# Kernel tuning notes

Measured on AMD Instinct MI355X. Metric: run time of the kernel, lower is better.

The kernel has to match this reference:

```python
import jax, jax.numpy as jnp
import numpy as np

NEG_SLOPE = 0.1

def lrelu(x):
    return jnp.where(x > 0, x, NEG_SLOPE * x)

def conv3(x, w, b):
    # 3x3 conv, stride 1, pad 1, NCHW / OIHW
    y = jax.lax.conv_general_dilated(x, w, (1, 1), ((1, 1), (1, 1)),
                                     dimension_numbers=('NCHW', 'OIHW', 'NCHW'))
    return y + b[None, :, None, None]

def correlation(f1, f2, stride):
    # 7x7 windowed cost volume, displacements in {-3..3}*stride, zero pad, /C
    B, C, H, W = f1.shape
    pad = 3 * stride
    f1s = f1[:, :, ::stride, ::stride]                      # [B,C,Ho,Wo] (ceil)
    f2p = jnp.pad(f2, ((0, 0), (0, 0), (pad, pad), (pad, pad)))
    outs = []
    for dy in range(7):
        for dx in range(7):
            sl = f2p[:, :, dy * stride: dy * stride + H: stride,
                           dx * stride: dx * stride + W: stride]
            outs.append(jnp.sum(f1s * sl, axis=1))           # [B,Ho,Wo]
    return jnp.stack(outs, axis=1) / C                       # [B,49,Ho,Wo]

def apply_offset(offset):
    # offset: [B,2,H,W]; channel 0 = x displacement, 1 = y displacement
    B, _, H, W = offset.shape
    gx = jnp.arange(W, dtype=offset.dtype)[None, None, :] + offset[:, 0]
    gy = jnp.arange(H, dtype=offset.dtype)[None, :, None] + offset[:, 1]
    gx = gx / ((W - 1.0) / 2.0) - 1.0
    gy = gy / ((H - 1.0) / 2.0) - 1.0
    return jnp.stack([gx, gy], axis=-1)                      # [B,H,W,2]

def grid_sample(img, grid):
    # bilinear, padding_mode='border', align_corners=True
    B, C, H, W = img.shape
    x = jnp.clip((grid[..., 0] + 1.0) * 0.5 * (W - 1), 0.0, W - 1.0)
    y = jnp.clip((grid[..., 1] + 1.0) * 0.5 * (H - 1), 0.0, H - 1.0)
    x0 = jnp.floor(x); y0 = jnp.floor(y)
    wx = x - x0; wy = y - y0
    x0 = x0.astype(jnp.int32); y0 = y0.astype(jnp.int32)
    x1 = jnp.minimum(x0 + 1, W - 1); y1 = jnp.minimum(y0 + 1, H - 1)
    imgf = img.reshape(B, C, H * W)
    def gather(yy, xx):
        idx = (yy * W + xx).reshape(B, 1, H * W)
        g = jnp.take_along_axis(imgf, jnp.broadcast_to(idx, (B, C, H * W)), axis=2)
        return g.reshape(B, C, H, W)
    wx = wx[:, None]; wy = wy[:, None]
    return (gather(y0, x0) * (1 - wx) * (1 - wy) + gather(y0, x1) * wx * (1 - wy)
            + gather(y1, x0) * (1 - wx) * wy + gather(y1, x1) * wx * wy)

def setup_inputs() -> dict:
    key = jax.random.key(0)
    ks = jax.random.split(key, 12)
    B, C, H, W = 8, 256, 128, 96
    s = 0.05
    return {
        'feat1': jax.random.normal(ks[0], (B, C, H, W), jnp.float32),
        'feat2': jax.random.normal(ks[1], (B, C, H, W), jnp.float32),
        'w1': s * jax.random.normal(ks[2], (128, 49, 3, 3), jnp.float32),
        'b1': jnp.zeros((128,), jnp.float32),
        'w2': s * jax.random.normal(ks[3], (64, 128, 3, 3), jnp.float32),
        'b2': jnp.zeros((64,), jnp.float32),
        'w3': s * jax.random.normal(ks[4], (32, 64, 3, 3), jnp.float32),
        'b3': jnp.zeros((32,), jnp.float32),
        'w4': s * jax.random.normal(ks[5], (2, 32, 3, 3), jnp.float32),
        'b4': jnp.zeros((2,), jnp.float32),
        'stride': 1,
    }

def reference(feat1, feat2, w1, b1, w2, b2, w3, b3, w4, b4, stride):
    corr = lrelu(correlation(feat1, feat2, stride))          # [B,49,H,W]
    h = lrelu(conv3(corr, w1, b1))
    h = lrelu(conv3(h, w2, b2))
    h = lrelu(conv3(h, w3, b3))
    flow = conv3(h, w4, b4)                                  # [B,2,H,W]
    grid = apply_offset(flow)
    warped = grid_sample(feat2, grid)                        # [B,C,H,W]
    return warped
```

## Files before the change

### kernel.cpp

```cpp
#include <hip/hip_runtime.h>

constexpr int B_ = 8, C_ = 256, H_ = 128, W_ = 96;
constexpr int HW_ = H_ * W_;

typedef __bf16 bf16x8 __attribute__((ext_vector_type(8)));
typedef float f32x4 __attribute__((ext_vector_type(4)));

__device__ __forceinline__ float lrelu_f(float v) { return v > 0.f ? v : 0.1f * v; }
__device__ __forceinline__ ushort f2b(float v) {
    __bf16 h = (__bf16)v;
    return __builtin_bit_cast(ushort, h);
}
__device__ __forceinline__ float blo(unsigned u) {
    return __builtin_bit_cast(float, u << 16);
}
__device__ __forceinline__ float bhi(unsigned u) {
    return __builtin_bit_cast(float, u & 0xffff0000u);
}

constexpr int CR = 4;
constexpr int F2R = 12;
constexpr int CCH = 8;

__global__ __launch_bounds__(768)
void corr_kernel(const float* __restrict__ f1, const float* __restrict__ f2,
                 ushort* __restrict__ corr_nhwc)
{
    __shared__ __align__(16) float s2[F2R][CCH][128];
    __shared__ __align__(16) float s1[CCH][CR][96];

    const int tid = threadIdx.x;
    const int pxg = tid % 24;
    const int ty = (tid / 24) % CR;
    const int dy = tid / 96;
    const int x0 = pxg * 4;

    const int b = blockIdx.x >> 5;
    const int y0 = (blockIdx.x & 31) * CR;

    float acc[7][4];
#pragma unroll
    for (int j = 0; j < 7; j++)
#pragma unroll
        for (int k = 0; k < 4; k++) acc[j][k] = 0.f;

    const float* f1p = f1 + b * C_ * HW_;
    const float* f2p = f2 + b * C_ * HW_;

    for (int cc = 0; cc < C_; cc += CCH) {
        __syncthreads();
#pragma unroll
        for (int k = 0; k < 16; k++) {
            int e = k * 768 + tid;
            int col = e & 127;
            int c = (e >> 7) & 7;
            int r = e >> 10;
            int yg = y0 + r - 3;
            int xg = col - 3;
            bool valid = ((unsigned)yg < (unsigned)H_) && ((unsigned)xg < (unsigned)W_);
            int ygc = min(max(yg, 0), H_ - 1);
            int xgc = min(max(xg, 0), W_ - 1);
            float v = f2p[(cc + c) * HW_ + ygc * W_ + xgc];
            s2[r][c][col] = valid ? v : 0.f;
        }
#pragma unroll
        for (int k = 0; k < 4; k++) {
            int e = k * 768 + tid;
            int idx = e / 96;
            int col = e - idx * 96;
            int c = idx >> 2;
            int r = idx & 3;
            s1[c][r][col] = f1p[(cc + c) * HW_ + (y0 + r) * W_ + col];
        }
        __syncthreads();
#pragma unroll
        for (int c = 0; c < CCH; c++) {
            float4 v1 = *(const float4*)&s1[c][ty][x0];
            float v1a[4] = {v1.x, v1.y, v1.z, v1.w};
            const float* rp = &s2[ty + dy][c][x0];
            float4 a0 = *(const float4*)&rp[0];
            float4 a1 = *(const float4*)&rp[4];
            float4 a2 = *(const float4*)&rp[8];
            float iv[12] = {a0.x, a0.y, a0.z, a0.w, a1.x, a1.y, a1.z, a1.w,
                            a2.x, a2.y, a2.z, a2.w};
#pragma unroll
            for (int dx = 0; dx < 7; dx++)
#pragma unroll
                for (int p = 0; p < 4; p++)
                    acc[dx][p] += v1a[p] * iv[p + dx];
        }
    }

    __syncthreads();
    ushort* t = (ushort*)&s2[0][0][0];
    const float scale = 1.f / 256.f;
    if (dy < 7) {
#pragma unroll
        for (int dx = 0; dx < 7; dx++)
#pragma unroll
            for (int p = 0; p < 4; p++)
                t[(ty * 96 + x0 + p) * 64 + dy * 7 + dx] =
                    f2b(lrelu_f(acc[dx][p] * scale));
    } else {
#pragma unroll
        for (int p = 0; p < 4; p++)
            for (int c = 49; c < 64; c++)
                t[(ty * 96 + x0 + p) * 64 + c] = 0;
    }
    __syncthreads();
    const uint4* src = (const uint4*)t;
    uint4* dst = (uint4*)(corr_nhwc + (size_t)(b * HW_ + y0 * W_) * 64);
    for (int e = tid; e < 3072; e += 768) dst[e] = src[e];
}

template <int CIN, int COUT, int CIP>
__global__ __launch_bounds__(256)
void pack_w(const float* __restrict__ w, ushort* __restrict__ wpk)
{
    int i = blockIdx.x * 256 + threadIdx.x;
    if (i >= 9 * COUT * CIP) return;
    int ci = i % CIP;
    int t = i / CIP;
    int oc = t % COUT;
    int tap = t / COUT;
    float v = (ci < CIN) ? w[(oc * CIN + ci) * 9 + tap] : 0.f;
    wpk[i] = f2b(v);
}

template <int CIP, int COUT, int OCB, int XT, int XTILES>
__global__ __launch_bounds__(256)
void conv_mfma(const ushort* __restrict__ in, const ushort* __restrict__ wpk,
               const float* __restrict__ bias, ushort* __restrict__ out)
{
    constexpr int OCF = OCB / 16, PXF = XT / 16, COLS = XT + 2;
    constexpr int G = CIP / 8, KC = CIP / 32;
    __shared__ __align__(16) ushort sIn[6 * COLS * CIP];

    const int tid = threadIdx.x;
    const int lane = tid & 63;
    const int ty = tid >> 6;
    const int ln = lane & 15;
    const int lq = lane >> 4;

    const int gx = blockIdx.x;
    const int xt = gx % XTILES;
    const int yt = (gx / XTILES) % 32;
    const int b = gx / (XTILES * 32);
    const int oc0 = blockIdx.y * OCB;
    const int x0 = xt * XT;
    const int y0 = yt * 4;

    constexpr int NU = 6 * COLS * G;
    for (int e = tid; e < NU; e += 256) {
        int g = e & (G - 1);
        int pc = e / G;
        int col = pc % COLS;
        int rr = pc / COLS;
        int yg = y0 - 1 + rr;
        int xg = x0 - 1 + col;
        uint4 v = make_uint4(0, 0, 0, 0);
        if ((unsigned)yg < (unsigned)H_ && (unsigned)xg < (unsigned)W_)
            v = *(const uint4*)(in + ((size_t)(b * HW_ + yg * W_ + xg) * CIP + g * 8));
        int p = rr * COLS + col;
        *(uint4*)(sIn + (size_t)(p * G + (g ^ (p & 7))) * 8) = v;
    }
    __syncthreads();

    f32x4 acc[OCF][PXF];
#pragma unroll
    for (int of = 0; of < OCF; of++)
#pragma unroll
        for (int pf = 0; pf < PXF; pf++) {
            f32x4 z = {0.f, 0.f, 0.f, 0.f};
            acc[of][pf] = z;
        }

    const uint4* wq = (const uint4*)wpk;
    for (int kc = 0; kc < KC; kc++) {
        for (int tap = 0; tap < 9; tap++) {
            const int r = tap / 3, s = tap % 3;
            bf16x8 afr[OCF];
#pragma unroll
            for (int of = 0; of < OCF; of++) {
                int off = ((tap * COUT + oc0 + of * 16 + ln) * CIP + kc * 32 + lq * 8) >> 3;
                afr[of] = __builtin_bit_cast(bf16x8, wq[off]);
            }
#pragma unroll
            for (int pf = 0; pf < PXF; pf++) {
                int p = (ty + r) * COLS + (pf * 16 + ln + s);
                int g = kc * 4 + lq;
                uint4 bv = *(const uint4*)(sIn + (size_t)(p * G + (g ^ (p & 7))) * 8);
                bf16x8 bfr = __builtin_bit_cast(bf16x8, bv);
#pragma unroll
                for (int of = 0; of < OCF; of++)
                    acc[of][pf] = __builtin_amdgcn_mfma_f32_16x16x32_bf16(
                        afr[of], bfr, acc[of][pf], 0, 0, 0);
            }
        }
    }

    const int y = y0 + ty;
#pragma unroll
    for (int of = 0; of < OCF; of++) {
        int ocb = oc0 + of * 16 + lq * 4;
        float4 bv = *(const float4*)(bias + ocb);
        float bs[4] = {bv.x, bv.y, bv.z, bv.w};
#pragma unroll
        for (int pf = 0; pf < PXF; pf++) {
            int x = x0 + pf * 16 + ln;
            ushort4 pk;
            pk.x = f2b(lrelu_f(acc[of][pf][0] + bs[0]));
            pk.y = f2b(lrelu_f(acc[of][pf][1] + bs[1]));
            pk.z = f2b(lrelu_f(acc[of][pf][2] + bs[2]));
            pk.w = f2b(lrelu_f(acc[of][pf][3] + bs[3]));
            *(ushort4*)(out + ((size_t)(b * HW_ + y * W_ + x) * COUT + ocb)) = pk;
        }
    }
}

__global__ __launch_bounds__(256)
void conv4_kernel(const ushort* __restrict__ in, const float* __restrict__ wgt,
                  const float* __restrict__ bias, float* __restrict__ flow)
{
    __shared__ float s_w[2 * 9 * 32];
    const int tid = threadIdx.x;
    for (int e = tid; e < 576; e += 256) {
        int ci = e & 31;
        int t = e >> 5;
        int tap = t % 9;
        int oc = t / 9;
        s_w[e] = wgt[(oc * 32 + ci) * 9 + tap];
    }
    __syncthreads();

    int pix = blockIdx.x * 256 + tid;
    int b = pix / HW_;
    int rem = pix - b * HW_;
    int yy = rem / W_;
    int xx = rem - yy * W_;

    float a0 = bias[0], a1 = bias[1];
    for (int tap = 0; tap < 9; tap++) {
        int r = tap / 3, s = tap % 3;
        int yg = yy + r - 1, xg = xx + s - 1;
        if ((unsigned)yg >= (unsigned)H_ || (unsigned)xg >= (unsigned)W_) continue;
        const uint4* p = (const uint4*)(in + (size_t)(b * HW_ + yg * W_ + xg) * 32);
        const float* w0 = &s_w[(0 * 9 + tap) * 32];
        const float* w1 = &s_w[(1 * 9 + tap) * 32];
#pragma unroll
        for (int q = 0; q < 4; q++) {
            uint4 v = p[q];
            unsigned uu[4] = {v.x, v.y, v.z, v.w};
#pragma unroll
            for (int h = 0; h < 4; h++) {
                int ci = q * 8 + h * 2;
                float vl = blo(uu[h]), vh = bhi(uu[h]);
                a0 += vl * w0[ci] + vh * w0[ci + 1];
                a1 += vl * w1[ci] + vh * w1[ci + 1];
            }
        }
    }
    flow[(b * 2 + 0) * HW_ + rem] = a0;
    flow[(b * 2 + 1) * HW_ + rem] = a1;
}

__global__ __launch_bounds__(256)
void warp_kernel(const float* __restrict__ f2, const float* __restrict__ flow,
                 float* __restrict__ out)
{
    int pix = blockIdx.x * 256 + threadIdx.x;
    int b = pix / HW_;
    int rem = pix - b * HW_;
    int yy = rem / W_;
    int xx = rem - yy * W_;

    float fx = flow[(b * 2 + 0) * HW_ + rem];
    float fy = flow[(b * 2 + 1) * HW_ + rem];
    float xs = fminf(fmaxf((float)xx + fx, 0.f), (float)(W_ - 1));
    float ys = fminf(fmaxf((float)yy + fy, 0.f), (float)(H_ - 1));
    float x0f = floorf(xs), y0f = floorf(ys);
    int x0 = (int)x0f, y0 = (int)y0f;
    float wx = xs - x0f, wy = ys - y0f;
    int x1 = min(x0 + 1, W_ - 1), y1 = min(y0 + 1, H_ - 1);

    int i00 = y0 * W_ + x0, i01 = y0 * W_ + x1;
    int i10 = y1 * W_ + x0, i11 = y1 * W_ + x1;
    float w00 = (1.f - wx) * (1.f - wy), w01 = wx * (1.f - wy);
    float w10 = (1.f - wx) * wy, w11 = wx * wy;

    const float* base = f2 + b * C_ * HW_;
    float* ob = out + b * C_ * HW_ + rem;
#pragma unroll 4
    for (int c = 0; c < C_; c++) {
        const float* p = base + c * HW_;
        ob[c * HW_] = p[i00] * w00 + p[i01] * w01 + p[i10] * w10 + p[i11] * w11;
    }
}

extern "C" void kernel_launch(void* const* d_in, const int* in_sizes, int n_in,
                              void* d_out, int out_size, void* d_ws, size_t ws_size,
                              hipStream_t stream)
{
    (void)in_sizes; (void)n_in; (void)out_size; (void)ws_size;
    const float* feat1 = (const float*)d_in[0];
    const float* feat2 = (const float*)d_in[1];
    const float* w1 = (const float*)d_in[2];
    const float* b1 = (const float*)d_in[3];
    const float* w2 = (const float*)d_in[4];
    const float* b2 = (const float*)d_in[5];
    const float* w3 = (const float*)d_in[6];
    const float* b3 = (const float*)d_in[7];
    const float* w4 = (const float*)d_in[8];
    const float* b4 = (const float*)d_in[9];

    char* ws = (char*)d_ws;
    ushort* corr_nhwc = (ushort*)(ws);
    ushort* h1 = (ushort*)(ws + 12582912);
    ushort* h2 = (ushort*)(ws + 37748736);
    ushort* h3 = (ushort*)(ws + 50331648);
    float* flow = (float*)(ws + 56623104);
    ushort* wpk1 = (ushort*)(ws + 57409536);
    ushort* wpk2 = (ushort*)(ws + 57556992);
    ushort* wpk3 = (ushort*)(ws + 57704448);
    float* out = (float*)d_out;

    pack_w<49, 128, 64><<<288, 256, 0, stream>>>(w1, wpk1);
    pack_w<128, 64, 128><<<288, 256, 0, stream>>>(w2, wpk2);
    pack_w<64, 32, 64><<<72, 256, 0, stream>>>(w3, wpk3);

    corr_kernel<<<256, 768, 0, stream>>>(feat1, feat2, corr_nhwc);
    conv_mfma<64, 128, 64, 48, 2><<<dim3(512, 2), 256, 0, stream>>>(corr_nhwc, wpk1, b1, h1);
    conv_mfma<128, 64, 64, 32, 3><<<dim3(768, 1), 256, 0, stream>>>(h1, wpk2, b2, h2);
    conv_mfma<64, 32, 32, 48, 2><<<dim3(512, 1), 256, 0, stream>>>(h2, wpk3, b3, h3);
    conv4_kernel<<<384, 256, 0, stream>>>(h3, w4, b4, flow);
    warp_kernel<<<384, 256, 0, stream>>>(feat2, flow, out);
}
```

Baseline: 522.2 us.

## Prefetch correlation tiles into registers, shrink row tiles, split warp over channels

The correlation kernel now processes 2 output rows per block with 384 threads (512 blocks) instead of 4 rows with 768. It loads the next channel chunk of feat1/feat2 into registers while computing the current one, which overlaps global loads with FMA work. Global offsets are precomputed once, shared-memory strides are padded to cut bank conflicts, and a block-index swizzle spreads work across batches. The warp kernel is split into 4 channel groups to quadruple the grid, at the cost of recomputing the bilinear indices per group and using more registers in the correlation kernel.

```diff
diff --git a/kernel.cpp b/kernel.cpp
--- a/kernel.cpp
+++ b/kernel.cpp
@@ -18,81 +18,125 @@
     return __builtin_bit_cast(float, u & 0xffff0000u);
 }
 
-constexpr int CR = 4;
-constexpr int F2R = 12;
 constexpr int CCH = 8;
-
-__global__ __launch_bounds__(768)
+constexpr int ROWS = 8;
+constexpr int SCOLS = 108;
+constexpr int S2STR = 132;
+constexpr int S1STR = 100;
+constexpr int NS2 = ROWS * CCH * SCOLS;
+constexpr int NPT2 = NS2 / 384;
+constexpr int NS1 = CCH * 2 * 96;
+constexpr int NPT1 = NS1 / 384;
+
+__global__ __launch_bounds__(384)
 void corr_kernel(const float* __restrict__ f1, const float* __restrict__ f2,
                  ushort* __restrict__ corr_nhwc)
 {
-    __shared__ __align__(16) float s2[F2R][CCH][128];
-    __shared__ __align__(16) float s1[CCH][CR][96];
+    __shared__ __align__(16) float s2f[CCH * ROWS * S2STR];
+    __shared__ __align__(16) float s1f[CCH * 2 * S1STR];
 
     const int tid = threadIdx.x;
     const int pxg = tid % 24;
-    const int ty = (tid / 24) % CR;
-    const int dy = tid / 96;
+    const int ty = (tid / 24) & 1;
+    const int dy = tid / 48;
     const int x0 = pxg * 4;
 
-    const int b = blockIdx.x >> 5;
-    const int y0 = (blockIdx.x & 31) * CR;
-
-    float acc[7][4];
-#pragma unroll
-    for (int j = 0; j < 7; j++)
-#pragma unroll
-        for (int k = 0; k < 4; k++) acc[j][k] = 0.f;
+    const int bid = blockIdx.x;
+    const int wg = (bid & 7) * 64 + (bid >> 3);
+    const int b = wg >> 6;
+    const int y0 = (wg & 63) * 2;
+
+    int goff2[NPT2], la2[NPT2];
+    unsigned gm = 0;
+#pragma unroll
+    for (int i = 0; i < NPT2; i++) {
+        int e = tid + i * 384;
+        int col = e % SCOLS;
+        int idx = e / SCOLS;
+        int c = idx & (CCH - 1);
+        int rr = idx >> 3;
+        int yg = y0 + rr - 3;
+        int xg = col - 3;
+        bool v = ((unsigned)yg < (unsigned)H_) && ((unsigned)xg < (unsigned)W_);
+        gm |= (unsigned)v << i;
+        int ygc = min(max(yg, 0), H_ - 1);
+        int xgc = min(max(xg, 0), W_ - 1);
+        goff2[i] = c * HW_ + ygc * W_ + xgc;
+        la2[i] = (c * ROWS + rr) * S2STR + col;
+    }
+    int goff1[NPT1], la1[NPT1];
+#pragma unroll
+    for (int i = 0; i < NPT1; i++) {
+        int e = tid + i * 384;
+        int col = e % 96;
+        int idx = e / 96;
+        int c = idx >> 1;
+        int tt = idx & 1;
+        goff1[i] = c * HW_ + (y0 + tt) * W_ + col;
+        la1[i] = (c * 2 + tt) * S1STR + col;
+    }
 
     const float* f1p = f1 + b * C_ * HW_;
     const float* f2p = f2 + b * C_ * HW_;
 
+    float acc[7][4];
+#pragma unroll
+    for (int j = 0; j < 7; j++)
+#pragma unroll
+        for (int k = 0; k < 4; k++) acc[j][k] = 0.f;
+
+    float r2[NPT2], r1[NPT1];
+#pragma unroll
+    for (int i = 0; i < NPT2; i++) {
+        float v = f2p[goff2[i]];
+        r2[i] = ((gm >> i) & 1u) ? v : 0.f;
+    }
+#pragma unroll
+    for (int i = 0; i < NPT1; i++) r1[i] = f1p[goff1[i]];
+
     for (int cc = 0; cc < C_; cc += CCH) {
         __syncthreads();
 #pragma unroll
-        for (int k = 0; k < 16; k++) {
-            int e = k * 768 + tid;
-            int col = e & 127;
-            int c = (e >> 7) & 7;
-            int r = e >> 10;
-            int yg = y0 + r - 3;
-            int xg = col - 3;
-            bool valid = ((unsigned)yg < (unsigned)H_) && ((unsigned)xg < (unsigned)W_);
-            int ygc = min(max(yg, 0), H_ - 1);
-            int xgc = min(max(xg, 0), W_ - 1);
-            float v = f2p[(cc + c) * HW_ + ygc * W_ + xgc];
-            s2[r][c][col] = valid ? v : 0.f;
-        }
-#pragma unroll
-        for (int k = 0; k < 4; k++) {
-            int e = k * 768 + tid;
-            int idx = e / 96;
-            int col = e - idx * 96;
-            int c = idx >> 2;
-            int r = idx & 3;
-            s1[c][r][col] = f1p[(cc + c) * HW_ + (y0 + r) * W_ + col];
-        }
+        for (int i = 0; i < NPT2; i++) s2f[la2[i]] = r2[i];
+#pragma unroll
+        for (int i = 0; i < NPT1; i++) s1f[la1[i]] = r1[i];
         __syncthreads();
-#pragma unroll
-        for (int c = 0; c < CCH; c++) {
-            float4 v1 = *(const float4*)&s1[c][ty][x0];
-            float v1a[4] = {v1.x, v1.y, v1.z, v1.w};
-            const float* rp = &s2[ty + dy][c][x0];
-            float4 a0 = *(const float4*)&rp[0];
-            float4 a1 = *(const float4*)&rp[4];
-            float4 a2 = *(const float4*)&rp[8];
-            float iv[12] = {a0.x, a0.y, a0.z, a0.w, a1.x, a1.y, a1.z, a1.w,
-                            a2.x, a2.y, a2.z, a2.w};
-#pragma unroll
-            for (int dx = 0; dx < 7; dx++)
-#pragma unroll
-                for (int p = 0; p < 4; p++)
-                    acc[dx][p] += v1a[p] * iv[p + dx];
+
+        if (cc + CCH < C_) {
+            const float* f2n = f2p + (cc + CCH) * HW_;
+            const float* f1n = f1p + (cc + CCH) * HW_;
+#pragma unroll
+            for (int i = 0; i < NPT2; i++) {
+                float v = f2n[goff2[i]];
+                r2[i] = ((gm >> i) & 1u) ? v : 0.f;
+            }
+#pragma unroll
+            for (int i = 0; i < NPT1; i++) r1[i] = f1n[goff1[i]];
+        }
+
+        if (dy < 7) {
+            const int r = ty + dy;
+#pragma unroll
+            for (int c = 0; c < CCH; c++) {
+                float4 v1 = *(const float4*)&s1f[(c * 2 + ty) * S1STR + x0];
+                float v1a[4] = {v1.x, v1.y, v1.z, v1.w};
+                const float* rp = &s2f[(c * ROWS + r) * S2STR + x0];
+                float4 a0 = *(const float4*)&rp[0];
+                float4 a1 = *(const float4*)&rp[4];
+                float4 a2 = *(const float4*)&rp[8];
+                float iv[12] = {a0.x, a0.y, a0.z, a0.w, a1.x, a1.y, a1.z, a1.w,
+                                a2.x, a2.y, a2.z, a2.w};
+#pragma unroll
+                for (int dx = 0; dx < 7; dx++)
+#pragma unroll
+                    for (int p = 0; p < 4; p++)
+                        acc[dx][p] += v1a[p] * iv[p + dx];
+            }
         }
     }
 
     __syncthreads();
-    ushort* t = (ushort*)&s2[0][0][0];
+    ushort* t = (ushort*)s2f;
     const float scale = 1.f / 256.f;
     if (dy < 7) {
 #pragma unroll
@@ -110,7 +154,8 @@
     __syncthreads();
     const uint4* src = (const uint4*)t;
     uint4* dst = (uint4*)(corr_nhwc + (size_t)(b * HW_ + y0 * W_) * 64);
-    for (int e = tid; e < 3072; e += 768) dst[e] = src[e];
+#pragma unroll
+    for (int k = 0; k < 4; k++) dst[k * 384 + tid] = src[k * 384 + tid];
 }
 
 template <int CIN, int COUT, int CIP>
@@ -269,6 +314,7 @@
                  float* __restrict__ out)
 {
     int pix = blockIdx.x * 256 + threadIdx.x;
+    int cbase = blockIdx.y * 64;
     int b = pix / HW_;
     int rem = pix - b * HW_;
     int yy = rem / W_;
@@ -288,10 +334,10 @@
     float w00 = (1.f - wx) * (1.f - wy), w01 = wx * (1.f - wy);
     float w10 = (1.f - wx) * wy, w11 = wx * wy;
 
-    const float* base = f2 + b * C_ * HW_;
-    float* ob = out + b * C_ * HW_ + rem;
+    const float* base = f2 + (size_t)(b * C_ + cbase) * HW_;
+    float* ob = out + (size_t)(b * C_ + cbase) * HW_ + rem;
 #pragma unroll 4
-    for (int c = 0; c < C_; c++) {
+    for (int c = 0; c < 64; c++) {
         const float* p = base + c * HW_;
         ob[c * HW_] = p[i00] * w00 + p[i01] * w01 + p[i10] * w10 + p[i11] * w11;
     }
@@ -328,10 +374,10 @@
     pack_w<128, 64, 128><<<288, 256, 0, stream>>>(w2, wpk2);
     pack_w<64, 32, 64><<<72, 256, 0, stream>>>(w3, wpk3);
 
-    corr_kernel<<<256, 768, 0, stream>>>(feat1, feat2, corr_nhwc);
+    corr_kernel<<<512, 384, 0, stream>>>(feat1, feat2, corr_nhwc);
     conv_mfma<64, 128, 64, 48, 2><<<dim3(512, 2), 256, 0, stream>>>(corr_nhwc, wpk1, b1, h1);
     conv_mfma<128, 64, 64, 32, 3><<<dim3(768, 1), 256, 0, stream>>>(h1, wpk2, b2, h2);
     conv_mfma<64, 32, 32, 48, 2><<<dim3(512, 1), 256, 0, stream>>>(h2, wpk3, b3, h3);
     conv4_kernel<<<384, 256, 0, stream>>>(h3, w4, b4, flow);
-    warp_kernel<<<384, 256, 0, stream>>>(feat2, flow, out);
-}
+    warp_kernel<<<dim3(384, 4), 256, 0, stream>>>(feat2, flow, out);
+}
```

Result: slower. 557.8 us (+6.8%).

## Prefetch correlation tiles into registers and split warp kernel across channel groups

Applied to the files above, without the earlier changes.

The correlation kernel now precomputes global and LDS offsets once and holds the next channel chunk of feat1/feat2 in registers, loading it while the current chunk is computed. This is meant to hide global load latency behind the FMA loop. The launch bound also asks for 3 blocks per CU, which may limit registers and cause spills. The warp kernel gains a grid y-dimension of 4, each block handling 64 channels, to give 4x more blocks for latency hiding at the cost of redoing the flow and bilinear weight setup per channel group.

```diff
diff --git a/kernel.cpp b/kernel.cpp
--- a/kernel.cpp
+++ b/kernel.cpp
@@ -22,7 +22,7 @@
 constexpr int F2R = 12;
 constexpr int CCH = 8;
 
-__global__ __launch_bounds__(768)
+__global__ __launch_bounds__(768, 3)
 void corr_kernel(const float* __restrict__ f1, const float* __restrict__ f2,
                  ushort* __restrict__ corr_nhwc)
 {
@@ -38,6 +38,35 @@
     const int b = blockIdx.x >> 5;
     const int y0 = (blockIdx.x & 31) * CR;
 
+    int goff2[16], la2[16];
+    unsigned vm = 0;
+#pragma unroll
+    for (int k = 0; k < 16; k++) {
+        int e = k * 768 + tid;
+        int col = e & 127;
+        int c = (e >> 7) & 7;
+        int r = e >> 10;
+        int yg = y0 + r - 3;
+        int xg = col - 3;
+        bool valid = ((unsigned)yg < (unsigned)H_) && ((unsigned)xg < (unsigned)W_);
+        vm |= (unsigned)valid << k;
+        int ygc = min(max(yg, 0), H_ - 1);
+        int xgc = min(max(xg, 0), W_ - 1);
+        goff2[k] = c * HW_ + ygc * W_ + xgc;
+        la2[k] = (r * CCH + c) * 128 + col;
+    }
+    int goff1[4], la1[4];
+#pragma unroll
+    for (int k = 0; k < 4; k++) {
+        int e = k * 768 + tid;
+        int idx = e / 96;
+        int col = e - idx * 96;
+        int c = idx >> 2;
+        int r = idx & 3;
+        goff1[k] = c * HW_ + (y0 + r) * W_ + col;
+        la1[k] = (c * CR + r) * 96 + col;
+    }
+
     float acc[7][4];
 #pragma unroll
     for (int j = 0; j < 7; j++)
@@ -46,33 +75,33 @@
 
     const float* f1p = f1 + b * C_ * HW_;
     const float* f2p = f2 + b * C_ * HW_;
+    float* s2lin = &s2[0][0][0];
+    float* s1lin = &s1[0][0][0];
+
+    float r2[16], r1[4];
+#pragma unroll
+    for (int k = 0; k < 16; k++) r2[k] = f2p[goff2[k]];
+#pragma unroll
+    for (int k = 0; k < 4; k++) r1[k] = f1p[goff1[k]];
 
     for (int cc = 0; cc < C_; cc += CCH) {
         __syncthreads();
 #pragma unroll
-        for (int k = 0; k < 16; k++) {
-            int e = k * 768 + tid;
-            int col = e & 127;
-            int c = (e >> 7) & 7;
-            int r = e >> 10;
-            int yg = y0 + r - 3;
-            int xg = col - 3;
-            bool valid = ((unsigned)yg < (unsigned)H_) && ((unsigned)xg < (unsigned)W_);
-            int ygc = min(max(yg, 0), H_ - 1);
-            int xgc = min(max(xg, 0), W_ - 1);
-            float v = f2p[(cc + c) * HW_ + ygc * W_ + xgc];
-            s2[r][c][col] = valid ? v : 0.f;
-        }
-#pragma unroll
-        for (int k = 0; k < 4; k++) {
-            int e = k * 768 + tid;
-            int idx = e / 96;
-            int col = e - idx * 96;
-            int c = idx >> 2;
-            int r = idx & 3;
-            s1[c][r][col] = f1p[(cc + c) * HW_ + (y0 + r) * W_ + col];
-        }
+        for (int k = 0; k < 16; k++)
+            s2lin[la2[k]] = ((vm >> k) & 1u) ? r2[k] : 0.f;
+#pragma unroll
+        for (int k = 0; k < 4; k++) s1lin[la1[k]] = r1[k];
         __syncthreads();
+
+        if (cc + CCH < C_) {
+            const float* f2n = f2p + (cc + CCH) * HW_;
+            const float* f1n = f1p + (cc + CCH) * HW_;
+#pragma unroll
+            for (int k = 0; k < 16; k++) r2[k] = f2n[goff2[k]];
+#pragma unroll
+            for (int k = 0; k < 4; k++) r1[k] = f1n[goff1[k]];
+        }
+
 #pragma unroll
         for (int c = 0; c < CCH; c++) {
             float4 v1 = *(const float4*)&s1[c][ty][x0];
@@ -269,6 +298,7 @@
                  float* __restrict__ out)
 {
     int pix = blockIdx.x * 256 + threadIdx.x;
+    int cbase = blockIdx.y * 64;
     int b = pix / HW_;
     int rem = pix - b * HW_;
     int yy = rem / W_;
@@ -288,10 +318,10 @@
     float w00 = (1.f - wx) * (1.f - wy), w01 = wx * (1.f - wy);
     float w10 = (1.f - wx) * wy, w11 = wx * wy;
 
-    const float* base = f2 + b * C_ * HW_;
-    float* ob = out + b * C_ * HW_ + rem;
+    const float* base = f2 + (size_t)(b * C_ + cbase) * HW_;
+    float* ob = out + (size_t)(b * C_ + cbase) * HW_ + rem;
 #pragma unroll 4
-    for (int c = 0; c < C_; c++) {
+    for (int c = 0; c < 64; c++) {
         const float* p = base + c * HW_;
         ob[c * HW_] = p[i00] * w00 + p[i01] * w01 + p[i10] * w10 + p[i11] * w11;
     }
@@ -333,5 +363,5 @@
     conv_mfma<128, 64, 64, 32, 3><<<dim3(768, 1), 256, 0, stream>>>(h1, wpk2, b2, h2);
     conv_mfma<64, 32, 32, 48, 2><<<dim3(512, 1), 256, 0, stream>>>(h2, wpk3, b3, h3);
     conv4_kernel<<<384, 256, 0, stream>>>(h3, w4, b4, flow);
-    warp_kernel<<<384, 256, 0, stream>>>(feat2, flow, out);
-}
+    warp_kernel<<<dim3(384, 4), 256, 0, stream>>>(feat2, flow, out);
+}
```

Result: slower. 733.6 us (+40.5%).
